# Kernel tuning notes

Measured on AMD Instinct MI355X. Metric: run time of the kernel, lower is better.

Reference implementation:

```python
import jax, jax.numpy as jnp
import numpy as np

DMODEL = 1024
N_EXPERTS = 8
EXPERT_SIZE = 4096
TOPK = 2
B, S = 2, 2048


def setup_inputs() -> dict:
    key = jax.random.key(0)
    ks = jax.random.split(key, 6)
    std = EXPERT_SIZE ** (-0.5)  # init_expert_weights: normal(0, expert_size**-0.5 * weight_scale)
    x = jax.random.normal(ks[0], (B, S, DMODEL), dtype=jnp.float32)
    gate_w = 0.02 * jax.random.normal(ks[1], (N_EXPERTS, DMODEL), dtype=jnp.float32)
    w1 = std * jax.random.normal(ks[2], (N_EXPERTS, EXPERT_SIZE, DMODEL), dtype=jnp.float32)
    b1 = jnp.zeros((N_EXPERTS, EXPERT_SIZE), dtype=jnp.float32)
    w2 = std * jax.random.normal(ks[3], (N_EXPERTS, DMODEL, EXPERT_SIZE), dtype=jnp.float32)
    b2 = jnp.zeros((N_EXPERTS, DMODEL), dtype=jnp.float32)
    return {"x": x, "gate_w": gate_w, "w1": w1, "b1": b1, "w2": w2, "b2": b2}


def reference(x, gate_w, w1, b1, w2, b2):
    # Router: gate linear (no bias) -> softmax -> top-k expert selection
    logits = jnp.einsum('bsd,ed->bse', x, gate_w)          # [B,S,E]
    probs = jax.nn.softmax(logits, axis=-1)                # gate_softmax
    top_w, top_i = jax.lax.top_k(probs, TOPK)              # [B,S,K]
    # Scatter top-k weights back to a dense [B,S,E] routing matrix
    route = jnp.sum(jax.nn.one_hot(top_i, N_EXPERTS, dtype=probs.dtype)
                    * top_w[..., None], axis=-2)           # [B,S,E]
    # Per-expert 2-layer MLP (Linear -> ReLU -> Linear), combined by route weights
    out = jnp.zeros_like(x)
    for e in range(N_EXPERTS):
        h = jax.nn.relu(jnp.einsum('bsd,hd->bsh', x, w1[e]) + b1[e])  # [B,S,H]
        y = jnp.einsum('bsh,dh->bsd', h, w2[e]) + b2[e]               # [B,S,D]
        out = out + route[..., e, None] * y
    return out
```

## Files before the change

kernel.cpp:

```cpp
#include <hip/hip_runtime.h>
#include <hip/hip_bf16.h>
#include <stdint.h>

#define DMODEL 1024
#define NEXP   8
#define HSZ    4096
#define NTOK   4096
#define KSPLIT 2

typedef __attribute__((ext_vector_type(8))) short bf16x8;
typedef __attribute__((ext_vector_type(4))) float f32x4;

__device__ __forceinline__ unsigned short f2bf(float f) {
  union { float f; unsigned u; } v; v.f = f;
  return (unsigned short)((v.u + 0x8000u) >> 16);
}

__device__ __forceinline__ void gl2lds16(const void* g, void* lds) {
  __builtin_amdgcn_global_load_lds(
      (const __attribute__((address_space(1))) unsigned*)g,
      (__attribute__((address_space(3))) unsigned*)lds, 16, 0, 0);
}

__global__ __launch_bounds__(256) void cvt_all_kernel(
    const float* __restrict__ w1, const float* __restrict__ w2,
    unsigned short* __restrict__ w1b, unsigned short* __restrict__ w2b) {
  const size_t n1 = (size_t)NEXP * HSZ * DMODEL / 4;
  size_t i = (size_t)blockIdx.x * 256 + threadIdx.x;
  const float* src; unsigned short* dst; size_t j;
  if (i < n1) { src = w1; dst = w1b; j = i; }
  else        { src = w2; dst = w2b; j = i - n1; }
  float4 v = ((const float4*)src)[j];
  ((ushort4*)dst)[j] = make_ushort4(f2bf(v.x), f2bf(v.y), f2bf(v.z), f2bf(v.w));
}

__global__ __launch_bounds__(256) void router_kernel(
    const float* __restrict__ x, const float* __restrict__ gw,
    int* __restrict__ cnt, int* __restrict__ tokl, float* __restrict__ twgt,
    int* __restrict__ sidx, unsigned short* __restrict__ xb) {
  __shared__ int lcnt[NEXP];
  __shared__ int lbase[NEXP];
  __shared__ int rE[32];
  __shared__ int rS[32];
  __shared__ float rW[32];
  const int tid = threadIdx.x;
  const int wave = tid >> 6;
  const int lane = tid & 63;
  if (tid < NEXP) lcnt[tid] = 0;
  __syncthreads();

  for (int i = 0; i < 4; ++i) {
    int lt = wave * 4 + i;
    int t = blockIdx.x * 16 + lt;
    const float* xr = x + (size_t)t * DMODEL;
    unsigned short* xbr = xb + (size_t)t * DMODEL;
    float acc[NEXP];
#pragma unroll
    for (int e = 0; e < NEXP; ++e) acc[e] = 0.f;
    for (int d = lane; d < DMODEL; d += 64) {
      float xv = xr[d];
      xbr[d] = f2bf(xv);
#pragma unroll
      for (int e = 0; e < NEXP; ++e) acc[e] = fmaf(xv, gw[e * DMODEL + d], acc[e]);
    }
#pragma unroll
    for (int e = 0; e < NEXP; ++e) {
#pragma unroll
      for (int o = 32; o > 0; o >>= 1) acc[e] += __shfl_down(acc[e], o);
    }
    if (lane == 0) {
      float m = acc[0];
#pragma unroll
      for (int e = 1; e < NEXP; ++e) m = fmaxf(m, acc[e]);
      float p[NEXP]; float s = 0.f;
#pragma unroll
      for (int e = 0; e < NEXP; ++e) { p[e] = __expf(acc[e] - m); s += p[e]; }
      float inv = 1.f / s;
      int i0 = 0; float b0 = p[0];
#pragma unroll
      for (int e = 1; e < NEXP; ++e) if (p[e] > b0) { b0 = p[e]; i0 = e; }
      int i1 = (i0 == 0) ? 1 : 0; float b1v = p[i1];
#pragma unroll
      for (int e = 0; e < NEXP; ++e) if (e != i0 && p[e] > b1v) { b1v = p[e]; i1 = e; }
      int s0l = atomicAdd(&lcnt[i0], 1);
      rE[lt * 2] = i0; rS[lt * 2] = s0l; rW[lt * 2] = b0 * inv;
      int s1l = atomicAdd(&lcnt[i1], 1);
      rE[lt * 2 + 1] = i1; rS[lt * 2 + 1] = s1l; rW[lt * 2 + 1] = b1v * inv;
    }
  }
  __syncthreads();
  if (tid < NEXP) lbase[tid] = atomicAdd(&cnt[tid], lcnt[tid]);
  __syncthreads();
  if (tid < 32) {
    int e = rE[tid];
    int p = lbase[e] + rS[tid];
    int t = blockIdx.x * 16 + (tid >> 1);
    tokl[e * NTOK + p] = t;
    twgt[e * NTOK + p] = rW[tid];
    sidx[2 * t + (tid & 1)] = (e << 16) | p;
  }
}

__global__ __launch_bounds__(256) void gemm1_bf_kernel(
    const unsigned short* __restrict__ Xbf, const unsigned short* __restrict__ W1bf,
    const float* __restrict__ b1, const int* __restrict__ cnt,
    const int* __restrict__ tokl, unsigned short* __restrict__ Hbuf) {
  const int e = blockIdx.z;
  const int ne = cnt[e];
  const int m0 = blockIdx.y * 128;
  if (m0 >= ne) return;
  const int n0 = blockIdx.x * 128;
  int toff = 0;
  for (int i = 0; i < NEXP; ++i) toff += (i < e) ? cnt[i] : 0;

  __shared__ __align__(16) unsigned short As[3][128 * 32];
  __shared__ __align__(16) unsigned short Bs[3][128 * 32];

  const int tid = threadIdx.x;
  const int lane = tid & 63;
  const int wave = tid >> 6;
  const int wm = (wave >> 1) * 64;
  const int wn = (wave & 1) * 64;

  const int srow = wave * 16 + (lane >> 2);
  const int scol = (((lane & 3) ^ ((lane >> 3) & 3)) << 3);
  const int* tlist = tokl + e * NTOK;
  const unsigned short* gA[2]; const unsigned short* gB[2];
  int lofs[2];
#pragma unroll
  for (int c = 0; c < 2; ++c) {
    int r = c * 64 + srow;
    int gr = m0 + r;
    int tk = tlist[(gr < ne) ? gr : 0];
    gA[c] = Xbf + (size_t)tk * DMODEL + scol;
    gB[c] = W1bf + (size_t)e * HSZ * DMODEL + (size_t)(n0 + r) * DMODEL + scol;
    lofs[c] = (c * 64 + wave * 16) * 32;
  }

  f32x4 acc[4][4];
#pragma unroll
  for (int i = 0; i < 4; ++i)
#pragma unroll
    for (int j = 0; j < 4; ++j) acc[i][j] = (f32x4){0.f, 0.f, 0.f, 0.f};

  const int fr = lane & 15;
  const int cb = lane >> 4;
  int aoff[4], boff[4];
#pragma unroll
  for (int i = 0; i < 4; ++i) {
    int ar = wm + i * 16 + fr;
    aoff[i] = ar * 32 + ((cb ^ ((ar >> 1) & 3)) << 3);
    int br = wn + i * 16 + fr;
    boff[i] = br * 32 + ((cb ^ ((br >> 1) & 3)) << 3);
  }

  constexpr int NSTEP = DMODEL / 32;
#pragma unroll
  for (int c = 0; c < 2; ++c) {
    gl2lds16(gA[c], &As[0][lofs[c]]);
    gl2lds16(gB[c], &Bs[0][lofs[c]]);
  }
#pragma unroll
  for (int c = 0; c < 2; ++c) {
    gl2lds16(gA[c] + 32, &As[1][lofs[c]]);
    gl2lds16(gB[c] + 32, &Bs[1][lofs[c]]);
  }

  int buf = 0;
  for (int t = 0; t < NSTEP; ++t) {
    int nb = buf + 2; if (nb >= 3) nb -= 3;
    if (t + 2 < NSTEP) {
      const int s = (t + 2) * 32;
#pragma unroll
      for (int c = 0; c < 2; ++c) {
        gl2lds16(gA[c] + s, &As[nb][lofs[c]]);
        gl2lds16(gB[c] + s, &Bs[nb][lofs[c]]);
      }
      asm volatile("s_waitcnt vmcnt(8)" ::: "memory");
    } else if (t + 1 < NSTEP) {
      asm volatile("s_waitcnt vmcnt(4)" ::: "memory");
    } else {
      asm volatile("s_waitcnt vmcnt(0)" ::: "memory");
    }
    __builtin_amdgcn_s_barrier();

    bf16x8 af[4], bfg[4];
#pragma unroll
    for (int i = 0; i < 4; ++i) {
      af[i]  = *(const bf16x8*)&As[buf][aoff[i]];
      bfg[i] = *(const bf16x8*)&Bs[buf][boff[i]];
    }
#pragma unroll
    for (int i = 0; i < 4; ++i)
#pragma unroll
      for (int j = 0; j < 4; ++j)
        acc[i][j] = __builtin_amdgcn_mfma_f32_16x16x32_bf16(bfg[j], af[i], acc[i][j], 0, 0, 0);
    __builtin_amdgcn_s_barrier();
    buf = (buf == 2) ? 0 : buf + 1;
  }

  const int hq = (lane >> 4) * 4;
#pragma unroll
  for (int i = 0; i < 4; ++i) {
    int trow = m0 + wm + i * 16 + fr;
    if (trow >= ne) continue;
    size_t hrow = (size_t)(toff + trow) * HSZ;
#pragma unroll
    for (int j = 0; j < 4; ++j) {
      int hcol = n0 + wn + j * 16 + hq;
      const float* bp = b1 + e * HSZ + hcol;
      unsigned short u[4];
#pragma unroll
      for (int r = 0; r < 4; ++r)
        u[r] = f2bf(fmaxf(acc[i][j][r] + bp[r], 0.f));
      *(ushort4*)&Hbuf[hrow + hcol] = make_ushort4(u[0], u[1], u[2], u[3]);
    }
  }
}

__global__ __launch_bounds__(256) void gemm2_bf_kernel(
    const unsigned short* __restrict__ Hbuf, const unsigned short* __restrict__ W2bf,
    const int* __restrict__ cnt, const float* __restrict__ twgt,
    float* __restrict__ Ybuf) {
  const int e = blockIdx.z & 7;
  const int ks = blockIdx.z >> 3;
  const int ne = cnt[e];
  const int m0 = blockIdx.y * 128;
  if (m0 >= ne) return;
  const int n0 = blockIdx.x * 128;
  const int kbase = ks * (HSZ / KSPLIT);
  int toff = 0;
  for (int i = 0; i < NEXP; ++i) toff += (i < e) ? cnt[i] : 0;

  __shared__ __align__(16) unsigned short As[3][128 * 32];
  __shared__ __align__(16) unsigned short Bs[3][128 * 32];

  const int tid = threadIdx.x;
  const int lane = tid & 63;
  const int wave = tid >> 6;
  const int wm = (wave >> 1) * 64;
  const int wn = (wave & 1) * 64;

  const int srow = wave * 16 + (lane >> 2);
  const int scol = (((lane & 3) ^ ((lane >> 3) & 3)) << 3);
  const unsigned short* gA[2]; const unsigned short* gB[2];
  int lofs[2];
#pragma unroll
  for (int c = 0; c < 2; ++c) {
    int r = c * 64 + srow;
    int gr = m0 + r;
    int rc = (gr < ne) ? gr : 0;
    gA[c] = Hbuf + (size_t)(toff + rc) * HSZ + kbase + scol;
    gB[c] = W2bf + (size_t)e * DMODEL * HSZ + (size_t)(n0 + r) * HSZ + kbase + scol;
    lofs[c] = (c * 64 + wave * 16) * 32;
  }

  f32x4 acc[4][4];
#pragma unroll
  for (int i = 0; i < 4; ++i)
#pragma unroll
    for (int j = 0; j < 4; ++j) acc[i][j] = (f32x4){0.f, 0.f, 0.f, 0.f};

  const int fr = lane & 15;
  const int cb = lane >> 4;
  int aoff[4], boff[4];
#pragma unroll
  for (int i = 0; i < 4; ++i) {
    int ar = wm + i * 16 + fr;
    aoff[i] = ar * 32 + ((cb ^ ((ar >> 1) & 3)) << 3);
    int br = wn + i * 16 + fr;
    boff[i] = br * 32 + ((cb ^ ((br >> 1) & 3)) << 3);
  }

  constexpr int NSTEP = (HSZ / KSPLIT) / 32;
#pragma unroll
  for (int c = 0; c < 2; ++c) {
    gl2lds16(gA[c], &As[0][lofs[c]]);
    gl2lds16(gB[c], &Bs[0][lofs[c]]);
  }
#pragma unroll
  for (int c = 0; c < 2; ++c) {
    gl2lds16(gA[c] + 32, &As[1][lofs[c]]);
    gl2lds16(gB[c] + 32, &Bs[1][lofs[c]]);
  }

  int buf = 0;
  for (int t = 0; t < NSTEP; ++t) {
    int nb = buf + 2; if (nb >= 3) nb -= 3;
    if (t + 2 < NSTEP) {
      const int s = (t + 2) * 32;
#pragma unroll
      for (int c = 0; c < 2; ++c) {
        gl2lds16(gA[c] + s, &As[nb][lofs[c]]);
        gl2lds16(gB[c] + s, &Bs[nb][lofs[c]]);
      }
      asm volatile("s_waitcnt vmcnt(8)" ::: "memory");
    } else if (t + 1 < NSTEP) {
      asm volatile("s_waitcnt vmcnt(4)" ::: "memory");
    } else {
      asm volatile("s_waitcnt vmcnt(0)" ::: "memory");
    }
    __builtin_amdgcn_s_barrier();

    bf16x8 af[4], bfg[4];
#pragma unroll
    for (int i = 0; i < 4; ++i) {
      af[i]  = *(const bf16x8*)&As[buf][aoff[i]];
      bfg[i] = *(const bf16x8*)&Bs[buf][boff[i]];
    }
#pragma unroll
    for (int i = 0; i < 4; ++i)
#pragma unroll
      for (int j = 0; j < 4; ++j)
        acc[i][j] = __builtin_amdgcn_mfma_f32_16x16x32_bf16(bfg[j], af[i], acc[i][j], 0, 0, 0);
    __builtin_amdgcn_s_barrier();
    buf = (buf == 2) ? 0 : buf + 1;
  }

  const float* wlist = twgt + e * NTOK;
  const int dq = (lane >> 4) * 4;
  float* yp = Ybuf + (size_t)ks * (2 * NTOK) * DMODEL;
#pragma unroll
  for (int i = 0; i < 4; ++i) {
    int trow = m0 + wm + i * 16 + fr;
    if (trow >= ne) continue;
    float wgt = wlist[trow];
    float* yrow = yp + (size_t)(toff + trow) * DMODEL;
#pragma unroll
    for (int j = 0; j < 4; ++j) {
      int d0 = n0 + wn + j * 16 + dq;
      float4 v = make_float4(wgt * acc[i][j][0], wgt * acc[i][j][1],
                             wgt * acc[i][j][2], wgt * acc[i][j][3]);
      *(float4*)(yrow + d0) = v;
    }
  }
}

__global__ __launch_bounds__(256) void combine_kernel(
    const float* __restrict__ Ybuf, const float* __restrict__ b2,
    const int* __restrict__ cnt, const int* __restrict__ sidx,
    const float* __restrict__ twgt, float* __restrict__ out) {
  int t = blockIdx.x;
  int offv[NEXP];
  int s = 0;
#pragma unroll
  for (int e = 0; e < NEXP; ++e) { offv[e] = s; s += cnt[e]; }
  int s0 = sidx[2 * t], s1 = sidx[2 * t + 1];
  int e0 = s0 >> 16, e1 = s1 >> 16;
  int sl0 = s0 & 0xffff, sl1 = s1 & 0xffff;
  size_t r0 = (size_t)(offv[e0] + sl0) * DMODEL;
  size_t r1 = (size_t)(offv[e1] + sl1) * DMODEL;
  float w0 = twgt[e0 * NTOK + sl0];
  float w1 = twgt[e1 * NTOK + sl1];
  const size_t PSTR = (size_t)(2 * NTOK) * DMODEL;
  int c = threadIdx.x * 4;
  float4 a0 = *(const float4*)(Ybuf + r0 + c);
  float4 a1 = *(const float4*)(Ybuf + PSTR + r0 + c);
  float4 c0 = *(const float4*)(Ybuf + r1 + c);
  float4 c1 = *(const float4*)(Ybuf + PSTR + r1 + c);
  float4 bb0 = *(const float4*)(b2 + (size_t)e0 * DMODEL + c);
  float4 bb1 = *(const float4*)(b2 + (size_t)e1 * DMODEL + c);
  *(float4*)(out + (size_t)t * DMODEL + c) = make_float4(
      a0.x + a1.x + c0.x + c1.x + w0 * bb0.x + w1 * bb1.x,
      a0.y + a1.y + c0.y + c1.y + w0 * bb0.y + w1 * bb1.y,
      a0.z + a1.z + c0.z + c1.z + w0 * bb0.z + w1 * bb1.z,
      a0.w + a1.w + c0.w + c1.w + w0 * bb0.w + w1 * bb1.w);
}

extern "C" void kernel_launch(void* const* d_in, const int* in_sizes, int n_in,
                              void* d_out, int out_size, void* d_ws, size_t ws_size,
                              hipStream_t stream) {
  const float* x  = (const float*)d_in[0];
  const float* gw = (const float*)d_in[1];
  const float* w1 = (const float*)d_in[2];
  const float* b1 = (const float*)d_in[3];
  const float* w2 = (const float*)d_in[4];
  const float* b2 = (const float*)d_in[5];
  float* out = (float*)d_out;

  char* ws = (char*)d_ws;
  int* cnt    = (int*)ws;
  int* tokl   = (int*)(ws + 128);
  float* twgt = (float*)(ws + 128 + NEXP * NTOK * 4);
  int* sidx   = (int*)(ws + 128 + 2 * NEXP * NTOK * 4);

  constexpr size_t OFF_XBF  = 327680;
  constexpr size_t OFF_W1BF = OFF_XBF  + (size_t)NTOK * DMODEL * 2;
  constexpr size_t OFF_W2BF = OFF_W1BF + (size_t)NEXP * HSZ * DMODEL * 2;
  constexpr size_t OFF_HBUF = OFF_W2BF + (size_t)NEXP * DMODEL * HSZ * 2;
  unsigned short* Xbf  = (unsigned short*)(ws + OFF_XBF);
  unsigned short* W1bf = (unsigned short*)(ws + OFF_W1BF);
  unsigned short* W2bf = (unsigned short*)(ws + OFF_W2BF);
  unsigned short* Hbuf = (unsigned short*)(ws + OFF_HBUF);
  float* Ybuf = (float*)(ws + OFF_W1BF);

  hipMemsetAsync(cnt, 0, 32, stream);
  router_kernel<<<NTOK / 16, 256, 0, stream>>>(x, gw, cnt, tokl, twgt, sidx, Xbf);
  const size_t ncvt = 2 * (size_t)NEXP * HSZ * DMODEL / 4;
  cvt_all_kernel<<<(unsigned)((ncvt + 255) / 256), 256, 0, stream>>>(
      w1, w2, W1bf, W2bf);
  gemm1_bf_kernel<<<dim3(HSZ / 128, NTOK / 128, NEXP), 256, 0, stream>>>(
      Xbf, W1bf, b1, cnt, tokl, Hbuf);
  gemm2_bf_kernel<<<dim3(DMODEL / 128, NTOK / 128, NEXP * KSPLIT), 256, 0, stream>>>(
      Hbuf, W2bf, cnt, twgt, Ybuf);
  combine_kernel<<<NTOK, 256, 0, stream>>>(Ybuf, b2, cnt, sidx, twgt, out);
}
```

Measured before the change: 605.9 us.

## Rewrite expert GEMMs as 256x256 tiles with 8 waves and interleaved ping-pong staging

Both expert GEMM kernels move from 128x128 tiles with 4 waves and a 3-stage K=32 pipeline to 256x256 tiles with 8 waves and a double-buffered K=64 pipeline in 128KB of LDS. Each K-tile is split into four quadrant phases that interleave LDS fragment reads, asynchronous global-to-LDS staging of future tiles and MFMA bursts. The bursts are wrapped in s_setprio and sched_barrier. The aim is more operand reuse per loaded byte and better overlap of memory traffic with matrix math. The cost is far fewer workgroups per expert (so more waste on partially filled M tiles), one block per CU, and fragile manual vmcnt accounting.

Result: faster. 578.7 us (-4.5%).

```diff
diff --git a/kernel.cpp b/kernel.cpp
--- a/kernel.cpp
+++ b/kernel.cpp
@@ -101,237 +101,265 @@
   }
 }
 
-__global__ __launch_bounds__(256) void gemm1_bf_kernel(
+
+#define SOFF(buf, mat, half) (((buf) * 4 + (mat) * 2 + (half)) * 8192)
+
+#define STG_A(buf, half, kt) do { if ((kt) < NSTEP) {                         \
+    gl2lds16(aP[half][0] + (size_t)(kt) * 64, &SH[SOFF(buf,0,half) + (w*16)*64]);     \
+    gl2lds16(aP[half][1] + (size_t)(kt) * 64, &SH[SOFF(buf,0,half) + (w*16+8)*64]); } } while(0)
+
+#define STG_B(buf, half, kt) do { if ((kt) < NSTEP) {                         \
+    gl2lds16(bP + (size_t)((half)*128) * Bstr + (size_t)(kt) * 64, &SH[SOFF(buf,1,half) + (w*16)*64]);   \
+    gl2lds16(bP + (size_t)((half)*128+8) * Bstr + (size_t)(kt) * 64, &SH[SOFF(buf,1,half) + (w*16+8)*64]); } } while(0)
+
+#define RD_A(dst, buf, half) do {                                             \
+    dst[0][0] = *(const bf16x8*)&SH[SOFF(buf,0,half) + aoff[0][0]];           \
+    dst[0][1] = *(const bf16x8*)&SH[SOFF(buf,0,half) + aoff[0][1]];           \
+    dst[1][0] = *(const bf16x8*)&SH[SOFF(buf,0,half) + aoff[1][0]];           \
+    dst[1][1] = *(const bf16x8*)&SH[SOFF(buf,0,half) + aoff[1][1]]; } while(0)
+
+#define RD_B(dst, buf, half) do {                                             \
+    _Pragma("unroll") for (int j_ = 0; j_ < 4; ++j_) {                        \
+      dst[j_][0] = *(const bf16x8*)&SH[SOFF(buf,1,half) + boff[j_][0]];       \
+      dst[j_][1] = *(const bf16x8*)&SH[SOFF(buf,1,half) + boff[j_][1]]; } } while(0)
+
+#define MFMA_Q(q, a, b) do {                                                  \
+    _Pragma("unroll") for (int i_ = 0; i_ < 2; ++i_)                          \
+    _Pragma("unroll") for (int j_ = 0; j_ < 4; ++j_)                          \
+    _Pragma("unroll") for (int k_ = 0; k_ < 2; ++k_)                          \
+      acc[q][i_][j_] = __builtin_amdgcn_mfma_f32_16x16x32_bf16(               \
+          b[j_][k_], a[i_][k_], acc[q][i_][j_], 0, 0, 0); } while(0)
+
+#define PH_COMPUTE(q, a, b)                                                   \
+    __builtin_amdgcn_s_barrier();                                             \
+    asm volatile("s_waitcnt lgkmcnt(0)" ::: "memory");                        \
+    __builtin_amdgcn_sched_barrier(0);                                        \
+    __builtin_amdgcn_s_setprio(1);                                            \
+    MFMA_Q(q, a, b);                                                          \
+    __builtin_amdgcn_s_setprio(0);                                            \
+    __builtin_amdgcn_sched_barrier(0);                                        \
+    __builtin_amdgcn_s_barrier();
+
+#define KTILE(buf, t) do {                                                    \
+                                                             \
+    RD_A(a0f, buf, 0); RD_B(b0f, buf, 0);                                     \
+    STG_B(buf ^ 1, 1, (t) + 1);                                               \
+    PH_COMPUTE(0, a0f, b0f)                                                   \
+                                                             \
+    RD_B(b1f, buf, 1);                                                        \
+    STG_A(buf, 0, (t) + 2);                                                   \
+    PH_COMPUTE(1, a0f, b1f)                                                   \
+                                                             \
+    RD_A(a1f, buf, 1);                                                        \
+    STG_B(buf, 0, (t) + 2);                                                   \
+    PH_COMPUTE(2, a1f, b0f)                                                   \
+                                            \
+    STG_A(buf, 1, (t) + 2);                                                   \
+    __builtin_amdgcn_s_barrier();                                             \
+    asm volatile("s_waitcnt lgkmcnt(0)" ::: "memory");                        \
+    __builtin_amdgcn_sched_barrier(0);                                        \
+    __builtin_amdgcn_s_setprio(1);                                            \
+    MFMA_Q(3, a1f, b1f);                                                      \
+    __builtin_amdgcn_s_setprio(0);                                            \
+    __builtin_amdgcn_sched_barrier(0);                                        \
+    if ((t) < NSTEP - 2) asm volatile("s_waitcnt vmcnt(6)" ::: "memory");     \
+    else                 asm volatile("s_waitcnt vmcnt(0)" ::: "memory");     \
+    __builtin_amdgcn_s_barrier();                                             \
+  } while(0)
+
+#define GEMM_PROLOGUE()                                                       \
+    STG_A(0, 0, 0); STG_B(0, 0, 0); STG_A(0, 1, 0); STG_B(0, 1, 0);           \
+    STG_A(1, 0, 1); STG_B(1, 0, 1); STG_A(1, 1, 1);                           \
+    asm volatile("s_waitcnt vmcnt(6)" ::: "memory");                          \
+    __builtin_amdgcn_s_barrier();
+
+__global__ __launch_bounds__(512) void gemm1_bf_kernel(
     const unsigned short* __restrict__ Xbf, const unsigned short* __restrict__ W1bf,
     const float* __restrict__ b1, const int* __restrict__ cnt,
     const int* __restrict__ tokl, unsigned short* __restrict__ Hbuf) {
   const int e = blockIdx.z;
   const int ne = cnt[e];
-  const int m0 = blockIdx.y * 128;
+  const int m0 = blockIdx.y * 256;
   if (m0 >= ne) return;
-  const int n0 = blockIdx.x * 128;
+  const int n0 = blockIdx.x * 256;
   int toff = 0;
   for (int i = 0; i < NEXP; ++i) toff += (i < e) ? cnt[i] : 0;
 
-  __shared__ __align__(16) unsigned short As[3][128 * 32];
-  __shared__ __align__(16) unsigned short Bs[3][128 * 32];
+  __shared__ __align__(16) unsigned short SH[65536];
 
   const int tid = threadIdx.x;
   const int lane = tid & 63;
-  const int wave = tid >> 6;
-  const int wm = (wave >> 1) * 64;
-  const int wn = (wave & 1) * 64;
-
-  const int srow = wave * 16 + (lane >> 2);
-  const int scol = (((lane & 3) ^ ((lane >> 3) & 3)) << 3);
+  const int w = tid >> 6;
+  const int aw = w >> 1;
+  const int bw = w & 1;
+  const int fr = lane & 15;
+  const int cb0 = lane >> 4;
+
+  constexpr int NSTEP = DMODEL / 64;
+  const size_t Bstr = DMODEL;
+
+  const int srow8 = lane >> 3;
+  const int sswz = ((lane & 7) ^ srow8) * 8;
   const int* tlist = tokl + e * NTOK;
-  const unsigned short* gA[2]; const unsigned short* gB[2];
-  int lofs[2];
-#pragma unroll
-  for (int c = 0; c < 2; ++c) {
-    int r = c * 64 + srow;
-    int gr = m0 + r;
-    int tk = tlist[(gr < ne) ? gr : 0];
-    gA[c] = Xbf + (size_t)tk * DMODEL + scol;
-    gB[c] = W1bf + (size_t)e * HSZ * DMODEL + (size_t)(n0 + r) * DMODEL + scol;
-    lofs[c] = (c * 64 + wave * 16) * 32;
-  }
-
-  f32x4 acc[4][4];
-#pragma unroll
-  for (int i = 0; i < 4; ++i)
-#pragma unroll
-    for (int j = 0; j < 4; ++j) acc[i][j] = (f32x4){0.f, 0.f, 0.f, 0.f};
-
-  const int fr = lane & 15;
-  const int cb = lane >> 4;
-  int aoff[4], boff[4];
-#pragma unroll
-  for (int i = 0; i < 4; ++i) {
-    int ar = wm + i * 16 + fr;
-    aoff[i] = ar * 32 + ((cb ^ ((ar >> 1) & 3)) << 3);
-    int br = wn + i * 16 + fr;
-    boff[i] = br * 32 + ((cb ^ ((br >> 1) & 3)) << 3);
-  }
-
-  constexpr int NSTEP = DMODEL / 32;
-#pragma unroll
-  for (int c = 0; c < 2; ++c) {
-    gl2lds16(gA[c], &As[0][lofs[c]]);
-    gl2lds16(gB[c], &Bs[0][lofs[c]]);
-  }
-#pragma unroll
-  for (int c = 0; c < 2; ++c) {
-    gl2lds16(gA[c] + 32, &As[1][lofs[c]]);
-    gl2lds16(gB[c] + 32, &Bs[1][lofs[c]]);
-  }
-
-  int buf = 0;
-  for (int t = 0; t < NSTEP; ++t) {
-    int nb = buf + 2; if (nb >= 3) nb -= 3;
-    if (t + 2 < NSTEP) {
-      const int s = (t + 2) * 32;
-#pragma unroll
-      for (int c = 0; c < 2; ++c) {
-        gl2lds16(gA[c] + s, &As[nb][lofs[c]]);
-        gl2lds16(gB[c] + s, &Bs[nb][lofs[c]]);
+  const unsigned short* aP[2][2];
+#pragma unroll
+  for (int h = 0; h < 2; ++h)
+#pragma unroll
+    for (int c = 0; c < 2; ++c) {
+      int gr = m0 + h * 128 + w * 16 + c * 8 + srow8;
+      int tk = tlist[(gr < ne) ? gr : 0];
+      aP[h][c] = Xbf + (size_t)tk * DMODEL + sswz;
+    }
+  const unsigned short* bP = W1bf + (size_t)e * HSZ * DMODEL
+      + (size_t)(n0 + w * 16 + srow8) * DMODEL + sswz;
+
+  int aoff[2][2], boff[4][2];
+#pragma unroll
+  for (int i = 0; i < 2; ++i)
+#pragma unroll
+    for (int kk = 0; kk < 2; ++kk) {
+      int rr = aw * 32 + i * 16 + fr;
+      aoff[i][kk] = rr * 64 + (((kk * 4 + cb0) ^ (fr & 7)) * 8);
+    }
+#pragma unroll
+  for (int j = 0; j < 4; ++j)
+#pragma unroll
+    for (int kk = 0; kk < 2; ++kk) {
+      int rr = bw * 64 + j * 16 + fr;
+      boff[j][kk] = rr * 64 + (((kk * 4 + cb0) ^ (fr & 7)) * 8);
+    }
+
+  f32x4 acc[4][2][4];
+#pragma unroll
+  for (int q = 0; q < 4; ++q)
+#pragma unroll
+    for (int i = 0; i < 2; ++i)
+#pragma unroll
+      for (int j = 0; j < 4; ++j) acc[q][i][j] = (f32x4){0.f, 0.f, 0.f, 0.f};
+
+  bf16x8 a0f[2][2], a1f[2][2], b0f[4][2], b1f[4][2];
+
+  GEMM_PROLOGUE()
+  for (int t = 0; t < NSTEP; t += 2) {
+    KTILE(0, t);
+    KTILE(1, t + 1);
+  }
+
+  const int dq = cb0 * 4;
+#pragma unroll
+  for (int q = 0; q < 4; ++q) {
+    const int qm = q >> 1, qn = q & 1;
+#pragma unroll
+    for (int i = 0; i < 2; ++i) {
+      int trow = m0 + qm * 128 + aw * 32 + i * 16 + fr;
+      if (trow >= ne) continue;
+      size_t hrow = (size_t)(toff + trow) * HSZ;
+#pragma unroll
+      for (int j = 0; j < 4; ++j) {
+        int hcol = n0 + qn * 128 + bw * 64 + j * 16 + dq;
+        const float* bp = b1 + e * HSZ + hcol;
+        unsigned short u[4];
+#pragma unroll
+        for (int r = 0; r < 4; ++r)
+          u[r] = f2bf(fmaxf(acc[q][i][j][r] + bp[r], 0.f));
+        *(ushort4*)&Hbuf[hrow + hcol] = make_ushort4(u[0], u[1], u[2], u[3]);
       }
-      asm volatile("s_waitcnt vmcnt(8)" ::: "memory");
-    } else if (t + 1 < NSTEP) {
-      asm volatile("s_waitcnt vmcnt(4)" ::: "memory");
-    } else {
-      asm volatile("s_waitcnt vmcnt(0)" ::: "memory");
-    }
-    __builtin_amdgcn_s_barrier();
-
-    bf16x8 af[4], bfg[4];
-#pragma unroll
-    for (int i = 0; i < 4; ++i) {
-      af[i]  = *(const bf16x8*)&As[buf][aoff[i]];
-      bfg[i] = *(const bf16x8*)&Bs[buf][boff[i]];
-    }
-#pragma unroll
-    for (int i = 0; i < 4; ++i)
-#pragma unroll
-      for (int j = 0; j < 4; ++j)
-        acc[i][j] = __builtin_amdgcn_mfma_f32_16x16x32_bf16(bfg[j], af[i], acc[i][j], 0, 0, 0);
-    __builtin_amdgcn_s_barrier();
-    buf = (buf == 2) ? 0 : buf + 1;
-  }
-
-  const int hq = (lane >> 4) * 4;
-#pragma unroll
-  for (int i = 0; i < 4; ++i) {
-    int trow = m0 + wm + i * 16 + fr;
-    if (trow >= ne) continue;
-    size_t hrow = (size_t)(toff + trow) * HSZ;
-#pragma unroll
-    for (int j = 0; j < 4; ++j) {
-      int hcol = n0 + wn + j * 16 + hq;
-      const float* bp = b1 + e * HSZ + hcol;
-      unsigned short u[4];
-#pragma unroll
-      for (int r = 0; r < 4; ++r)
-        u[r] = f2bf(fmaxf(acc[i][j][r] + bp[r], 0.f));
-      *(ushort4*)&Hbuf[hrow + hcol] = make_ushort4(u[0], u[1], u[2], u[3]);
-    }
-  }
-}
-
-__global__ __launch_bounds__(256) void gemm2_bf_kernel(
+    }
+  }
+}
+
+__global__ __launch_bounds__(512) void gemm2_bf_kernel(
     const unsigned short* __restrict__ Hbuf, const unsigned short* __restrict__ W2bf,
     const int* __restrict__ cnt, const float* __restrict__ twgt,
     float* __restrict__ Ybuf) {
   const int e = blockIdx.z & 7;
   const int ks = blockIdx.z >> 3;
   const int ne = cnt[e];
-  const int m0 = blockIdx.y * 128;
+  const int m0 = blockIdx.y * 256;
   if (m0 >= ne) return;
-  const int n0 = blockIdx.x * 128;
+  const int n0 = blockIdx.x * 256;
   const int kbase = ks * (HSZ / KSPLIT);
   int toff = 0;
   for (int i = 0; i < NEXP; ++i) toff += (i < e) ? cnt[i] : 0;
 
-  __shared__ __align__(16) unsigned short As[3][128 * 32];
-  __shared__ __align__(16) unsigned short Bs[3][128 * 32];
+  __shared__ __align__(16) unsigned short SH[65536];
 
   const int tid = threadIdx.x;
   const int lane = tid & 63;
-  const int wave = tid >> 6;
-  const int wm = (wave >> 1) * 64;
-  const int wn = (wave & 1) * 64;
-
-  const int srow = wave * 16 + (lane >> 2);
-  const int scol = (((lane & 3) ^ ((lane >> 3) & 3)) << 3);
-  const unsigned short* gA[2]; const unsigned short* gB[2];
-  int lofs[2];
-#pragma unroll
-  for (int c = 0; c < 2; ++c) {
-    int r = c * 64 + srow;
-    int gr = m0 + r;
-    int rc = (gr < ne) ? gr : 0;
-    gA[c] = Hbuf + (size_t)(toff + rc) * HSZ + kbase + scol;
-    gB[c] = W2bf + (size_t)e * DMODEL * HSZ + (size_t)(n0 + r) * HSZ + kbase + scol;
-    lofs[c] = (c * 64 + wave * 16) * 32;
-  }
-
-  f32x4 acc[4][4];
-#pragma unroll
-  for (int i = 0; i < 4; ++i)
-#pragma unroll
-    for (int j = 0; j < 4; ++j) acc[i][j] = (f32x4){0.f, 0.f, 0.f, 0.f};
-
+  const int w = tid >> 6;
+  const int aw = w >> 1;
+  const int bw = w & 1;
   const int fr = lane & 15;
-  const int cb = lane >> 4;
-  int aoff[4], boff[4];
-#pragma unroll
-  for (int i = 0; i < 4; ++i) {
-    int ar = wm + i * 16 + fr;
-    aoff[i] = ar * 32 + ((cb ^ ((ar >> 1) & 3)) << 3);
-    int br = wn + i * 16 + fr;
-    boff[i] = br * 32 + ((cb ^ ((br >> 1) & 3)) << 3);
-  }
-
-  constexpr int NSTEP = (HSZ / KSPLIT) / 32;
-#pragma unroll
-  for (int c = 0; c < 2; ++c) {
-    gl2lds16(gA[c], &As[0][lofs[c]]);
-    gl2lds16(gB[c], &Bs[0][lofs[c]]);
-  }
-#pragma unroll
-  for (int c = 0; c < 2; ++c) {
-    gl2lds16(gA[c] + 32, &As[1][lofs[c]]);
-    gl2lds16(gB[c] + 32, &Bs[1][lofs[c]]);
-  }
-
-  int buf = 0;
-  for (int t = 0; t < NSTEP; ++t) {
-    int nb = buf + 2; if (nb >= 3) nb -= 3;
-    if (t + 2 < NSTEP) {
-      const int s = (t + 2) * 32;
-#pragma unroll
-      for (int c = 0; c < 2; ++c) {
-        gl2lds16(gA[c] + s, &As[nb][lofs[c]]);
-        gl2lds16(gB[c] + s, &Bs[nb][lofs[c]]);
+  const int cb0 = lane >> 4;
+
+  constexpr int NSTEP = (HSZ / KSPLIT) / 64;
+  const size_t Bstr = HSZ;
+
+  const int srow8 = lane >> 3;
+  const int sswz = ((lane & 7) ^ srow8) * 8;
+  const unsigned short* aP[2][2];
+#pragma unroll
+  for (int h = 0; h < 2; ++h)
+#pragma unroll
+    for (int c = 0; c < 2; ++c) {
+      int gr = m0 + h * 128 + w * 16 + c * 8 + srow8;
+      int rc = (gr < ne) ? gr : 0;
+      aP[h][c] = Hbuf + (size_t)(toff + rc) * HSZ + kbase + sswz;
+    }
+  const unsigned short* bP = W2bf + (size_t)e * DMODEL * HSZ
+      + (size_t)(n0 + w * 16 + srow8) * HSZ + kbase + sswz;
+
+  int aoff[2][2], boff[4][2];
+#pragma unroll
+  for (int i = 0; i < 2; ++i)
+#pragma unroll
+    for (int kk = 0; kk < 2; ++kk) {
+      int rr = aw * 32 + i * 16 + fr;
+      aoff[i][kk] = rr * 64 + (((kk * 4 + cb0) ^ (fr & 7)) * 8);
+    }
+#pragma unroll
+  for (int j = 0; j < 4; ++j)
+#pragma unroll
+    for (int kk = 0; kk < 2; ++kk) {
+      int rr = bw * 64 + j * 16 + fr;
+      boff[j][kk] = rr * 64 + (((kk * 4 + cb0) ^ (fr & 7)) * 8);
+    }
+
+  f32x4 acc[4][2][4];
+#pragma unroll
+  for (int q = 0; q < 4; ++q)
+#pragma unroll
+    for (int i = 0; i < 2; ++i)
+#pragma unroll
+      for (int j = 0; j < 4; ++j) acc[q][i][j] = (f32x4){0.f, 0.f, 0.f, 0.f};
+
+  bf16x8 a0f[2][2], a1f[2][2], b0f[4][2], b1f[4][2];
+
+  GEMM_PROLOGUE()
+  for (int t = 0; t < NSTEP; t += 2) {
+    KTILE(0, t);
+    KTILE(1, t + 1);
+  }
+
+  const float* wlist = twgt + e * NTOK;
+  float* yp = Ybuf + (size_t)ks * (2 * NTOK) * DMODEL;
+  const int dq = cb0 * 4;
+#pragma unroll
+  for (int q = 0; q < 4; ++q) {
+    const int qm = q >> 1, qn = q & 1;
+#pragma unroll
+    for (int i = 0; i < 2; ++i) {
+      int trow = m0 + qm * 128 + aw * 32 + i * 16 + fr;
+      if (trow >= ne) continue;
+      float wgt = wlist[trow];
+      float* yrow = yp + (size_t)(toff + trow) * DMODEL;
+#pragma unroll
+      for (int j = 0; j < 4; ++j) {
+        int d0 = n0 + qn * 128 + bw * 64 + j * 16 + dq;
+        float4 v = make_float4(wgt * acc[q][i][j][0], wgt * acc[q][i][j][1],
+                               wgt * acc[q][i][j][2], wgt * acc[q][i][j][3]);
+        *(float4*)(yrow + d0) = v;
       }
-      asm volatile("s_waitcnt vmcnt(8)" ::: "memory");
-    } else if (t + 1 < NSTEP) {
-      asm volatile("s_waitcnt vmcnt(4)" ::: "memory");
-    } else {
-      asm volatile("s_waitcnt vmcnt(0)" ::: "memory");
-    }
-    __builtin_amdgcn_s_barrier();
-
-    bf16x8 af[4], bfg[4];
-#pragma unroll
-    for (int i = 0; i < 4; ++i) {
-      af[i]  = *(const bf16x8*)&As[buf][aoff[i]];
-      bfg[i] = *(const bf16x8*)&Bs[buf][boff[i]];
-    }
-#pragma unroll
-    for (int i = 0; i < 4; ++i)
-#pragma unroll
-      for (int j = 0; j < 4; ++j)
-        acc[i][j] = __builtin_amdgcn_mfma_f32_16x16x32_bf16(bfg[j], af[i], acc[i][j], 0, 0, 0);
-    __builtin_amdgcn_s_barrier();
-    buf = (buf == 2) ? 0 : buf + 1;
-  }
-
-  const float* wlist = twgt + e * NTOK;
-  const int dq = (lane >> 4) * 4;
-  float* yp = Ybuf + (size_t)ks * (2 * NTOK) * DMODEL;
-#pragma unroll
-  for (int i = 0; i < 4; ++i) {
-    int trow = m0 + wm + i * 16 + fr;
-    if (trow >= ne) continue;
-    float wgt = wlist[trow];
-    float* yrow = yp + (size_t)(toff + trow) * DMODEL;
-#pragma unroll
-    for (int j = 0; j < 4; ++j) {
-      int d0 = n0 + wn + j * 16 + dq;
-      float4 v = make_float4(wgt * acc[i][j][0], wgt * acc[i][j][1],
-                             wgt * acc[i][j][2], wgt * acc[i][j][3]);
-      *(float4*)(yrow + d0) = v;
     }
   }
 }
@@ -399,9 +427,9 @@
   const size_t ncvt = 2 * (size_t)NEXP * HSZ * DMODEL / 4;
   cvt_all_kernel<<<(unsigned)((ncvt + 255) / 256), 256, 0, stream>>>(
       w1, w2, W1bf, W2bf);
-  gemm1_bf_kernel<<<dim3(HSZ / 128, NTOK / 128, NEXP), 256, 0, stream>>>(
+  gemm1_bf_kernel<<<dim3(HSZ / 256, NTOK / 256, NEXP), 512, 0, stream>>>(
       Xbf, W1bf, b1, cnt, tokl, Hbuf);
-  gemm2_bf_kernel<<<dim3(DMODEL / 128, NTOK / 128, NEXP * KSPLIT), 256, 0, stream>>>(
+  gemm2_bf_kernel<<<dim3(DMODEL / 256, NTOK / 256, NEXP * KSPLIT), 512, 0, stream>>>(
       Hbuf, W2bf, cnt, twgt, Ybuf);
   combine_kernel<<<NTOK, 256, 0, stream>>>(Ybuf, b2, cnt, sidx, twgt, out);
 }
```
